# Kernel optimization log

Hardware: AMD Instinct MI355X
Metric: run time of the kernel (lower is better)

Reference implementation:

```python
import jax, jax.numpy as jnp
import numpy as np

N_NODES = 100000
K_STEPS = 10
ALPHA = 0.1


def setup_inputs() -> dict:
    key = jax.random.key(0)
    k1, k2, k3, k4 = jax.random.split(key, 4)
    x = jax.random.normal(k1, (N_NODES, 512), dtype=jnp.float32)
    edge_index = jax.random.randint(k2, (2, 3200000), 0, N_NODES, dtype=jnp.int64)
    W1 = jax.random.normal(k3, (512, 256), dtype=jnp.float32) * (1.0 / np.sqrt(512))
    b1 = jnp.zeros((256,), dtype=jnp.float32)
    W2 = jax.random.normal(k4, (256, 64), dtype=jnp.float32) * (1.0 / np.sqrt(256))
    b2 = jnp.zeros((64,), dtype=jnp.float32)
    return {"x": x, "edge_index": edge_index, "W1": W1, "b1": b1, "W2": W2, "b2": b2}


def _gcn_norm(edge_index, num_nodes):
    # Add self loops and compute symmetric normalization deg^-1/2 A deg^-1/2.
    loops = jnp.arange(num_nodes, dtype=edge_index.dtype)
    src = jnp.concatenate([edge_index[0], loops])
    dst = jnp.concatenate([edge_index[1], loops])
    deg = jax.ops.segment_sum(jnp.ones_like(dst, dtype=jnp.float32), dst,
                              num_segments=num_nodes)
    dinv = jnp.where(deg > 0, jax.lax.rsqrt(deg), 0.0)
    norm = dinv[src] * dinv[dst]  # [E + N]
    return src, dst, norm


def reference(x, edge_index, W1, b1, W2, b2):
    n = x.shape[0]
    # MLP (dropout is identity at inference)
    h = jax.nn.relu(x @ W1 + b1)
    h = h @ W2 + b2  # [N, C]
    # APPNP propagation: h_{k+1} = (1-alpha) * A_hat h_k + alpha * h_0
    src, dst, norm = _gcn_norm(edge_index, n)
    h0 = h

    def step(carry, _):
        msg = carry[src] * norm[:, None]                     # gather + scale
        agg = jax.ops.segment_sum(msg, dst, num_segments=n)  # scatter-add
        return (1.0 - ALPHA) * agg + ALPHA * h0, None

    h, _ = jax.lax.scan(step, h, None, length=K_STEPS)
    return jax.nn.log_softmax(h, axis=1)
```

## Files before the change

kernel.cpp:

```cpp
#include <hip/hip_runtime.h>
#include <cstdint>
#include <cstddef>


typedef _Float16 half8 __attribute__((ext_vector_type(8)));
typedef float floatx4 __attribute__((ext_vector_type(4)));

__device__ inline float2 unpack2(uint u) {
    union { uint u; _Float16 h[2]; } c; c.u = u;
    return make_float2((float)c.h[0], (float)c.h[1]);
}
__device__ inline uint pack2(float a, float b) {
    union { uint u; _Float16 h[2]; } c; c.h[0] = (_Float16)a; c.h[1] = (_Float16)b;
    return c.u;
}

__global__ void transpose_w1(const float* __restrict__ W1, _Float16* __restrict__ W1t) {
    int i = blockIdx.x * 256 + threadIdx.x;
    if (i < 512 * 256) {
        int k = i >> 8, c = i & 255;
        W1t[(size_t)c * 512 + k] = (_Float16)W1[i];
    }
}
__global__ void transpose_w2(const float* __restrict__ W2, _Float16* __restrict__ W2t) {
    int i = blockIdx.x * 256 + threadIdx.x;
    if (i < 256 * 64) {
        int k = i >> 6, c = i & 63;
        W2t[(size_t)c * 256 + k] = (_Float16)W2[i];
    }
}

__global__ __launch_bounds__(256) void mlp_kernel(
    const float* __restrict__ x, const _Float16* __restrict__ W1t,
    const float* __restrict__ b1, const _Float16* __restrict__ W2t,
    const float* __restrict__ b2, _Float16* __restrict__ h0h, int n)
{
    __shared__ __align__(16) _Float16 xs[32][520];
    __shared__ __align__(16) _Float16 hmid[32][264];

    const int tid  = threadIdx.x;
    const int lane = tid & 63;
    const int wid  = tid >> 6;
    const int r0blk = blockIdx.x * 32;
    const int lr = lane & 15;
    const int lg = lane >> 4;

    for (int fi = tid; fi < 32 * 128; fi += 256) {
        int r = fi >> 7, k4 = (fi & 127) * 4;
        float4 v = *(const float4*)(x + (size_t)(r0blk + r) * 512 + k4);
        union { short4 s; _Float16 h[4]; } c;
        c.h[0] = (_Float16)v.x; c.h[1] = (_Float16)v.y;
        c.h[2] = (_Float16)v.z; c.h[3] = (_Float16)v.w;
        *(short4*)&xs[r][k4] = c.s;
    }
    __syncthreads();

    const int wr = wid >> 1, wc = wid & 1;
    floatx4 acc1[8];
#pragma unroll
    for (int ct = 0; ct < 8; ++ct) {
        float b = b1[wc * 128 + ct * 16 + lr];
        acc1[ct] = (floatx4){b, b, b, b};
    }

#pragma unroll 2
    for (int kk = 0; kk < 512; kk += 32) {
        half8 a = *(const half8*)&xs[wr * 16 + lr][kk + lg * 8];
        half8 bfr[8];
#pragma unroll
        for (int ct = 0; ct < 8; ++ct)
            bfr[ct] = *(const half8*)&W1t[(size_t)(wc * 128 + ct * 16 + lr) * 512 + kk + lg * 8];
#pragma unroll
        for (int ct = 0; ct < 8; ++ct)
            acc1[ct] = __builtin_amdgcn_mfma_f32_16x16x32_f16(a, bfr[ct], acc1[ct], 0, 0, 0);
    }

#pragma unroll
    for (int ct = 0; ct < 8; ++ct) {
#pragma unroll
        for (int r = 0; r < 4; ++r) {
            float v = fmaxf(acc1[ct][r], 0.f);
            hmid[wr * 16 + lg * 4 + r][wc * 128 + ct * 16 + lr] = (_Float16)v;
        }
    }
    __syncthreads();

    const int rt = wid >> 1, ct2 = (wid & 1) * 2;
    floatx4 acc2[2] = {(floatx4){0,0,0,0}, (floatx4){0,0,0,0}};
#pragma unroll 2
    for (int kk = 0; kk < 256; kk += 32) {
        half8 a = *(const half8*)&hmid[rt * 16 + lr][kk + lg * 8];
#pragma unroll
        for (int q = 0; q < 2; ++q) {
            half8 b = *(const half8*)&W2t[(size_t)((ct2 + q) * 16 + lr) * 256 + kk + lg * 8];
            acc2[q] = __builtin_amdgcn_mfma_f32_16x16x32_f16(a, b, acc2[q], 0, 0, 0);
        }
    }
#pragma unroll
    for (int q = 0; q < 2; ++q) {
        int col = (ct2 + q) * 16 + lr;
        float bb = b2[col];
#pragma unroll
        for (int r = 0; r < 4; ++r) {
            int row = r0blk + rt * 16 + lg * 4 + r;
            h0h[(size_t)row * 64 + col] = (_Float16)(acc2[q][r] + bb);
        }
    }
}

__global__ void init_counts_kernel(int* __restrict__ counts, int n) {
    int i = blockIdx.x * blockDim.x + threadIdx.x;
    if (i < n) counts[i] = 1;
}

__global__ void count_kernel(const int* __restrict__ dstL, int* __restrict__ counts,
                             int e, int rs, int n) {
    const int r = blockIdx.x & 7;
    const int g = blockIdx.x >> 3;
    const int B = gridDim.x >> 3;
    const int lo = r * rs;
    const int hi = min(lo + rs, n);
    for (int i = g * blockDim.x + threadIdx.x; i < e; i += B * blockDim.x) {
        int d = dstL[i];
        if (d >= lo && d < hi) atomicAdd(&counts[d], 1);
    }
}

__global__ void dinv_kernel(const int* __restrict__ counts, float* __restrict__ dinv, int n) {
    int i = blockIdx.x * blockDim.x + threadIdx.x;
    if (i < n) dinv[i] = 1.0f / sqrtf((float)counts[i]);
}

__global__ __launch_bounds__(256) void scan_a(const int* __restrict__ counts,
                                              int* __restrict__ rowptr,
                                              int* __restrict__ bsums, int n)
{
    __shared__ int s[256];
    const int t = threadIdx.x;
    const int i = blockIdx.x * 256 + t;
    int v = (i < n) ? (counts[i] - 1) : 0;
    s[t] = v;
    __syncthreads();
    for (int off = 1; off < 256; off <<= 1) {
        int add = (t >= off) ? s[t - off] : 0;
        __syncthreads();
        s[t] += add;
        __syncthreads();
    }
    if (i < n) rowptr[i] = s[t] - v;
    if (t == 255) bsums[blockIdx.x] = s[255];
}

__global__ __launch_bounds__(512) void scan_b(const int* __restrict__ bsums,
                                              int* __restrict__ boff, int nb)
{
    __shared__ int s[512];
    const int t = threadIdx.x;
    int v = (t < nb) ? bsums[t] : 0;
    s[t] = v;
    __syncthreads();
    for (int off = 1; off < 512; off <<= 1) {
        int add = (t >= off) ? s[t - off] : 0;
        __syncthreads();
        s[t] += add;
        __syncthreads();
    }
    if (t < nb) boff[t] = s[t] - v;
}

__global__ __launch_bounds__(256) void scan_c(int* __restrict__ rowptr,
                                              int* __restrict__ cursor,
                                              const int* __restrict__ boff, int n, int e)
{
    int i = blockIdx.x * 256 + threadIdx.x;
    if (i < n) {
        int v = rowptr[i] + boff[blockIdx.x];
        rowptr[i] = v;
        cursor[i] = v;
    }
    if (i == 0) rowptr[n] = e;
}

__global__ void fill_kernel(const int* __restrict__ srcL, const int* __restrict__ dstL,
                            int* __restrict__ cursor, int* __restrict__ srcs,
                            int e, int rs, int n) {
    const int r = blockIdx.x & 7;
    const int g = blockIdx.x >> 3;
    const int B = gridDim.x >> 3;
    const int lo = r * rs;
    const int hi = min(lo + rs, n);
    for (int i = g * blockDim.x + threadIdx.x; i < e; i += B * blockDim.x) {
        int d = dstL[i];
        if (d >= lo && d < hi) {
            int pos = atomicAdd(&cursor[d], 1);
            srcs[pos] = srcL[i];
        }
    }
}

__global__ __launch_bounds__(256) void prop_kernel(
    const uint* __restrict__ hu, const uint* __restrict__ h0u,
    uint* __restrict__ hnu, const int* __restrict__ rowptr,
    const int* __restrict__ srcs, const float* __restrict__ dinv, int n)
{
    const int node = (blockIdx.x * blockDim.x + threadIdx.x) >> 6;
    if (node >= n) return;
    const int lane = threadIdx.x & 63;
    const int half_ = lane >> 5;
    const int p = lane & 31;
    const int e0 = rowptr[node], e1 = rowptr[node + 1];
    float accx = 0.f, accy = 0.f;
    int e = e0 + half_;
    for (; e + 6 < e1; e += 8) {
        int s0 = srcs[e], s1 = srcs[e + 2], s2 = srcs[e + 4], s3 = srcs[e + 6];
        float w0 = dinv[s0], w1 = dinv[s1], w2 = dinv[s2], w3 = dinv[s3];
        float2 f0 = unpack2(hu[(size_t)s0 * 32 + p]);
        float2 f1 = unpack2(hu[(size_t)s1 * 32 + p]);
        float2 f2 = unpack2(hu[(size_t)s2 * 32 + p]);
        float2 f3 = unpack2(hu[(size_t)s3 * 32 + p]);
        accx += w0 * f0.x; accy += w0 * f0.y;
        accx += w1 * f1.x; accy += w1 * f1.y;
        accx += w2 * f2.x; accy += w2 * f2.y;
        accx += w3 * f3.x; accy += w3 * f3.y;
    }
    for (; e < e1; e += 2) {
        int s = srcs[e];
        float w = dinv[s];
        float2 f = unpack2(hu[(size_t)s * 32 + p]);
        accx += w * f.x; accy += w * f.y;
    }
    accx += __shfl_xor(accx, 32);
    accy += __shfl_xor(accy, 32);

    const float di = dinv[node];
    float2 self = unpack2(hu[(size_t)node * 32 + p]);
    float2 anc  = unpack2(h0u[(size_t)node * 32 + p]);
    float ox = 0.9f * (di * accx + self.x * di * di) + 0.1f * anc.x;
    float oy = 0.9f * (di * accy + self.y * di * di) + 0.1f * anc.y;
    if (half_ == 0) hnu[(size_t)node * 32 + p] = pack2(ox, oy);
}

__global__ __launch_bounds__(256) void logsoftmax_kernel(
    const _Float16* __restrict__ h, float* __restrict__ out, int n)
{
    const int row = (blockIdx.x * blockDim.x + threadIdx.x) >> 6;
    const int lane = threadIdx.x & 63;
    if (row >= n) return;
    float v = (float)h[(size_t)row * 64 + lane];
    float m = v;
#pragma unroll
    for (int o = 32; o > 0; o >>= 1) m = fmaxf(m, __shfl_xor(m, o));
    float ex = expf(v - m);
    float s = ex;
#pragma unroll
    for (int o = 32; o > 0; o >>= 1) s += __shfl_xor(s, o);
    out[(size_t)row * 64 + lane] = v - m - logf(s);
}

extern "C" void kernel_launch(void* const* d_in, const int* in_sizes, int n_in,
                              void* d_out, int out_size, void* d_ws, size_t ws_size,
                              hipStream_t stream)
{
    const float* x  = (const float*)d_in[0];
    const int*   ei = (const int*)d_in[1];
    const float* W1 = (const float*)d_in[2];
    const float* b1 = (const float*)d_in[3];
    const float* W2 = (const float*)d_in[4];
    const float* b2 = (const float*)d_in[5];
    float* out = (float*)d_out;

    const int n = in_sizes[0] / 512;
    const int e = in_sizes[1] / 2;
    const int* srcL = ei;
    const int* dstL = ei + e;

    char* wsb = (char*)d_ws;
    size_t off = 0;
    auto alloc = [&](size_t bytes) -> void* {
        void* p = wsb + off;
        off = (off + bytes + 255) & ~(size_t)255;
        return p;
    };
    _Float16* h0h = (_Float16*)alloc((size_t)n * 64 * 2);
    _Float16* hp0 = (_Float16*)alloc((size_t)n * 64 * 2);
    _Float16* hp1 = (_Float16*)alloc((size_t)n * 64 * 2);
    int*   srcs   = (int*)alloc((size_t)e * 4);
    float* dinv   = (float*)alloc((size_t)n * 4);
    int*   counts = (int*)alloc((size_t)n * 4);
    int*   rowptr = (int*)alloc((size_t)(n + 1) * 4);
    int*   bsums  = (int*)alloc(4096);
    int*   boff   = (int*)alloc(4096);
    _Float16* W1t = (_Float16*)alloc((size_t)512 * 256 * 2);
    _Float16* W2t = (_Float16*)alloc((size_t)256 * 64 * 2);
    int* cursor = counts;

    const int nb = (n + 255) / 256;
    const int rs = (n + 7) / 8;

    transpose_w1<<<(512 * 256 + 255) / 256, 256, 0, stream>>>(W1, W1t);
    transpose_w2<<<(256 * 64 + 255) / 256, 256, 0, stream>>>(W2, W2t);

    mlp_kernel<<<n / 32, 256, 0, stream>>>(x, W1t, b1, W2t, b2, h0h, n);

    init_counts_kernel<<<nb, 256, 0, stream>>>(counts, n);
    count_kernel<<<1024, 256, 0, stream>>>(dstL, counts, e, rs, n);
    dinv_kernel<<<nb, 256, 0, stream>>>(counts, dinv, n);
    scan_a<<<nb, 256, 0, stream>>>(counts, rowptr, bsums, n);
    scan_b<<<1, 512, 0, stream>>>(bsums, boff, nb);
    scan_c<<<nb, 256, 0, stream>>>(rowptr, cursor, boff, n, e);
    fill_kernel<<<1024, 256, 0, stream>>>(srcL, dstL, cursor, srcs, e, rs, n);

    const int pgrid = (n * 64 + 255) / 256;
    const uint* hin = (const uint*)h0h;
    uint* bufs[2] = {(uint*)hp0, (uint*)hp1};
    for (int it = 0; it < 10; ++it) {
        uint* hn = bufs[it & 1];
        prop_kernel<<<pgrid, 256, 0, stream>>>(hin, (const uint*)h0h, hn,
                                               rowptr, srcs, dinv, n);
        hin = hn;
    }
    logsoftmax_kernel<<<pgrid, 256, 0, stream>>>((const _Float16*)hin, out, n);
}
```

Baseline: 1.588 ms.

## Propagate dinv-scaled features to drop per-edge dinv gathers; stage W1 through LDS

Reformulates the propagation in terms of g = D^{-1/2} h, so each edge contributes an unweighted sum and the per-edge dinv[src] gather goes away. A per-node coefficient 0.9/deg is precomputed, the MLP output is prescaled by dinv, and logsoftmax divides by dinv to recover h. The MLP kernel now streams W1 in a pre-tiled layout through double-buffered shared memory instead of reading it straight from global memory. This requires moving the MLP after the degree computation, and storing the scaled values in fp16 may change rounding behaviour.

Result: faster. 1.445 ms (-9.0%).

```diff
diff --git a/kernel.cpp b/kernel.cpp
--- a/kernel.cpp
+++ b/kernel.cpp
@@ -15,11 +15,11 @@
     return c.u;
 }
 
-__global__ void transpose_w1(const float* __restrict__ W1, _Float16* __restrict__ W1t) {
+__global__ void transpose_w1_tiled(const float* __restrict__ W1, _Float16* __restrict__ W1tt) {
     int i = blockIdx.x * 256 + threadIdx.x;
     if (i < 512 * 256) {
-        int k = i >> 8, c = i & 255;
-        W1t[(size_t)c * 512 + k] = (_Float16)W1[i];
+        int kt = i >> 13, c = (i >> 5) & 255, j = i & 31;
+        W1tt[i] = (_Float16)W1[(size_t)(kt * 32 + j) * 256 + c];
     }
 }
 __global__ void transpose_w2(const float* __restrict__ W2, _Float16* __restrict__ W2t) {
@@ -31,12 +31,13 @@
 }
 
 __global__ __launch_bounds__(256) void mlp_kernel(
-    const float* __restrict__ x, const _Float16* __restrict__ W1t,
+    const float* __restrict__ x, const _Float16* __restrict__ W1tt,
     const float* __restrict__ b1, const _Float16* __restrict__ W2t,
-    const float* __restrict__ b2, _Float16* __restrict__ h0h, int n)
+    const float* __restrict__ b2, const float* __restrict__ dinv,
+    _Float16* __restrict__ g0h, int n)
 {
     __shared__ __align__(16) _Float16 xs[32][520];
-    __shared__ __align__(16) _Float16 hmid[32][264];
+    __shared__ __align__(16) _Float16 wraw[2][10240];
 
     const int tid  = threadIdx.x;
     const int lane = tid & 63;
@@ -53,7 +54,6 @@
         c.h[2] = (_Float16)v.z; c.h[3] = (_Float16)v.w;
         *(short4*)&xs[r][k4] = c.s;
     }
-    __syncthreads();
 
     const int wr = wid >> 1, wc = wid & 1;
     floatx4 acc1[8];
@@ -63,18 +63,45 @@
         acc1[ct] = (floatx4){b, b, b, b};
     }
 
-#pragma unroll 2
-    for (int kk = 0; kk < 512; kk += 32) {
-        half8 a = *(const half8*)&xs[wr * 16 + lr][kk + lg * 8];
-        half8 bfr[8];
-#pragma unroll
-        for (int ct = 0; ct < 8; ++ct)
-            bfr[ct] = *(const half8*)&W1t[(size_t)(wc * 128 + ct * 16 + lr) * 512 + kk + lg * 8];
-#pragma unroll
-        for (int ct = 0; ct < 8; ++ct)
-            acc1[ct] = __builtin_amdgcn_mfma_f32_16x16x32_f16(a, bfr[ct], acc1[ct], 0, 0, 0);
-    }
-
+    const int sc = tid >> 2, ss = (tid & 3) * 8;
+    int4 st0, st1, st2, st3;
+    {
+        const int4* gs = (const int4*)(W1tt);
+        st0 = gs[tid]; st1 = gs[tid + 256]; st2 = gs[tid + 512]; st3 = gs[tid + 768];
+    }
+    {
+        _Float16* wb = wraw[0];
+        *(int4*)&wb[(sc +   0) * 40 + ss] = st0;
+        *(int4*)&wb[(sc +  64) * 40 + ss] = st1;
+        *(int4*)&wb[(sc + 128) * 40 + ss] = st2;
+        *(int4*)&wb[(sc + 192) * 40 + ss] = st3;
+    }
+    __syncthreads();
+
+    for (int kt = 0; kt < 16; ++kt) {
+        const int cur = kt & 1;
+        if (kt < 15) {
+            const int4* gs = (const int4*)(W1tt + (size_t)(kt + 1) * 8192);
+            st0 = gs[tid]; st1 = gs[tid + 256]; st2 = gs[tid + 512]; st3 = gs[tid + 768];
+        }
+        const _Float16* wb = wraw[cur];
+        half8 a = *(const half8*)&xs[wr * 16 + lr][kt * 32 + lg * 8];
+#pragma unroll
+        for (int ct = 0; ct < 8; ++ct) {
+            half8 b = *(const half8*)&wb[(wc * 128 + ct * 16 + lr) * 40 + lg * 8];
+            acc1[ct] = __builtin_amdgcn_mfma_f32_16x16x32_f16(a, b, acc1[ct], 0, 0, 0);
+        }
+        if (kt < 15) {
+            _Float16* wn = wraw[cur ^ 1];
+            *(int4*)&wn[(sc +   0) * 40 + ss] = st0;
+            *(int4*)&wn[(sc +  64) * 40 + ss] = st1;
+            *(int4*)&wn[(sc + 128) * 40 + ss] = st2;
+            *(int4*)&wn[(sc + 192) * 40 + ss] = st3;
+        }
+        __syncthreads();
+    }
+
+    _Float16 (*hmid)[264] = (_Float16(*)[264])&wraw[0][0];
 #pragma unroll
     for (int ct = 0; ct < 8; ++ct) {
 #pragma unroll
@@ -103,7 +130,8 @@
 #pragma unroll
         for (int r = 0; r < 4; ++r) {
             int row = r0blk + rt * 16 + lg * 4 + r;
-            h0h[(size_t)row * 64 + col] = (_Float16)(acc2[q][r] + bb);
+            float di = dinv[row];
+            g0h[(size_t)row * 64 + col] = (_Float16)(di * (acc2[q][r] + bb));
         }
     }
 }
@@ -126,9 +154,14 @@
     }
 }
 
-__global__ void dinv_kernel(const int* __restrict__ counts, float* __restrict__ dinv, int n) {
+__global__ void dinv_kernel(const int* __restrict__ counts, float* __restrict__ dinv,
+                            float* __restrict__ Anode, int n) {
     int i = blockIdx.x * blockDim.x + threadIdx.x;
-    if (i < n) dinv[i] = 1.0f / sqrtf((float)counts[i]);
+    if (i < n) {
+        float deg = (float)counts[i];
+        dinv[i] = 1.0f / sqrtf(deg);
+        Anode[i] = 0.9f / deg;
+    }
 }
 
 __global__ __launch_bounds__(256) void scan_a(const int* __restrict__ counts,
@@ -199,9 +232,9 @@
 }
 
 __global__ __launch_bounds__(256) void prop_kernel(
-    const uint* __restrict__ hu, const uint* __restrict__ h0u,
-    uint* __restrict__ hnu, const int* __restrict__ rowptr,
-    const int* __restrict__ srcs, const float* __restrict__ dinv, int n)
+    const uint* __restrict__ gu, const uint* __restrict__ g0u,
+    uint* __restrict__ gnu, const int* __restrict__ rowptr,
+    const int* __restrict__ srcs, const float* __restrict__ Anode, int n)
 {
     const int node = (blockIdx.x * blockDim.x + threadIdx.x) >> 6;
     if (node >= n) return;
@@ -213,40 +246,38 @@
     int e = e0 + half_;
     for (; e + 6 < e1; e += 8) {
         int s0 = srcs[e], s1 = srcs[e + 2], s2 = srcs[e + 4], s3 = srcs[e + 6];
-        float w0 = dinv[s0], w1 = dinv[s1], w2 = dinv[s2], w3 = dinv[s3];
-        float2 f0 = unpack2(hu[(size_t)s0 * 32 + p]);
-        float2 f1 = unpack2(hu[(size_t)s1 * 32 + p]);
-        float2 f2 = unpack2(hu[(size_t)s2 * 32 + p]);
-        float2 f3 = unpack2(hu[(size_t)s3 * 32 + p]);
-        accx += w0 * f0.x; accy += w0 * f0.y;
-        accx += w1 * f1.x; accy += w1 * f1.y;
-        accx += w2 * f2.x; accy += w2 * f2.y;
-        accx += w3 * f3.x; accy += w3 * f3.y;
+        float2 f0 = unpack2(gu[(size_t)s0 * 32 + p]);
+        float2 f1 = unpack2(gu[(size_t)s1 * 32 + p]);
+        float2 f2 = unpack2(gu[(size_t)s2 * 32 + p]);
+        float2 f3 = unpack2(gu[(size_t)s3 * 32 + p]);
+        accx += f0.x; accy += f0.y;
+        accx += f1.x; accy += f1.y;
+        accx += f2.x; accy += f2.y;
+        accx += f3.x; accy += f3.y;
     }
     for (; e < e1; e += 2) {
-        int s = srcs[e];
-        float w = dinv[s];
-        float2 f = unpack2(hu[(size_t)s * 32 + p]);
-        accx += w * f.x; accy += w * f.y;
+        float2 f = unpack2(gu[(size_t)srcs[e] * 32 + p]);
+        accx += f.x; accy += f.y;
     }
     accx += __shfl_xor(accx, 32);
     accy += __shfl_xor(accy, 32);
 
-    const float di = dinv[node];
-    float2 self = unpack2(hu[(size_t)node * 32 + p]);
-    float2 anc  = unpack2(h0u[(size_t)node * 32 + p]);
-    float ox = 0.9f * (di * accx + self.x * di * di) + 0.1f * anc.x;
-    float oy = 0.9f * (di * accy + self.y * di * di) + 0.1f * anc.y;
-    if (half_ == 0) hnu[(size_t)node * 32 + p] = pack2(ox, oy);
+    const float A = Anode[node];
+    float2 self = unpack2(gu[(size_t)node * 32 + p]);
+    float2 anc  = unpack2(g0u[(size_t)node * 32 + p]);
+    float ox = A * (accx + self.x) + 0.1f * anc.x;
+    float oy = A * (accy + self.y) + 0.1f * anc.y;
+    if (half_ == 0) gnu[(size_t)node * 32 + p] = pack2(ox, oy);
 }
 
 __global__ __launch_bounds__(256) void logsoftmax_kernel(
-    const _Float16* __restrict__ h, float* __restrict__ out, int n)
+    const _Float16* __restrict__ g, const float* __restrict__ dinv,
+    float* __restrict__ out, int n)
 {
     const int row = (blockIdx.x * blockDim.x + threadIdx.x) >> 6;
     const int lane = threadIdx.x & 63;
     if (row >= n) return;
-    float v = (float)h[(size_t)row * 64 + lane];
+    float v = (float)g[(size_t)row * 64 + lane] / dinv[row];
     float m = v;
 #pragma unroll
     for (int o = 32; o > 0; o >>= 1) m = fmaxf(m, __shfl_xor(m, o));
@@ -281,43 +312,44 @@
         off = (off + bytes + 255) & ~(size_t)255;
         return p;
     };
-    _Float16* h0h = (_Float16*)alloc((size_t)n * 64 * 2);
-    _Float16* hp0 = (_Float16*)alloc((size_t)n * 64 * 2);
-    _Float16* hp1 = (_Float16*)alloc((size_t)n * 64 * 2);
+    _Float16* g0h = (_Float16*)alloc((size_t)n * 64 * 2);
+    _Float16* gp0 = (_Float16*)alloc((size_t)n * 64 * 2);
+    _Float16* gp1 = (_Float16*)alloc((size_t)n * 64 * 2);
     int*   srcs   = (int*)alloc((size_t)e * 4);
     float* dinv   = (float*)alloc((size_t)n * 4);
+    float* Anode  = (float*)alloc((size_t)n * 4);
     int*   counts = (int*)alloc((size_t)n * 4);
     int*   rowptr = (int*)alloc((size_t)(n + 1) * 4);
     int*   bsums  = (int*)alloc(4096);
     int*   boff   = (int*)alloc(4096);
-    _Float16* W1t = (_Float16*)alloc((size_t)512 * 256 * 2);
-    _Float16* W2t = (_Float16*)alloc((size_t)256 * 64 * 2);
+    _Float16* W1tt = (_Float16*)alloc((size_t)512 * 256 * 2);
+    _Float16* W2t  = (_Float16*)alloc((size_t)256 * 64 * 2);
     int* cursor = counts;
 
     const int nb = (n + 255) / 256;
     const int rs = (n + 7) / 8;
 
-    transpose_w1<<<(512 * 256 + 255) / 256, 256, 0, stream>>>(W1, W1t);
+    transpose_w1_tiled<<<(512 * 256 + 255) / 256, 256, 0, stream>>>(W1, W1tt);
     transpose_w2<<<(256 * 64 + 255) / 256, 256, 0, stream>>>(W2, W2t);
-
-    mlp_kernel<<<n / 32, 256, 0, stream>>>(x, W1t, b1, W2t, b2, h0h, n);
 
     init_counts_kernel<<<nb, 256, 0, stream>>>(counts, n);
     count_kernel<<<1024, 256, 0, stream>>>(dstL, counts, e, rs, n);
-    dinv_kernel<<<nb, 256, 0, stream>>>(counts, dinv, n);
+    dinv_kernel<<<nb, 256, 0, stream>>>(counts, dinv, Anode, n);
     scan_a<<<nb, 256, 0, stream>>>(counts, rowptr, bsums, n);
     scan_b<<<1, 512, 0, stream>>>(bsums, boff, nb);
     scan_c<<<nb, 256, 0, stream>>>(rowptr, cursor, boff, n, e);
     fill_kernel<<<1024, 256, 0, stream>>>(srcL, dstL, cursor, srcs, e, rs, n);
 
+    mlp_kernel<<<n / 32, 256, 0, stream>>>(x, W1tt, b1, W2t, b2, dinv, g0h, n);
+
     const int pgrid = (n * 64 + 255) / 256;
-    const uint* hin = (const uint*)h0h;
-    uint* bufs[2] = {(uint*)hp0, (uint*)hp1};
+    const uint* gin = (const uint*)g0h;
+    uint* bufs[2] = {(uint*)gp0, (uint*)gp1};
     for (int it = 0; it < 10; ++it) {
-        uint* hn = bufs[it & 1];
-        prop_kernel<<<pgrid, 256, 0, stream>>>(hin, (const uint*)h0h, hn,
-                                               rowptr, srcs, dinv, n);
-        hin = hn;
-    }
-    logsoftmax_kernel<<<pgrid, 256, 0, stream>>>((const _Float16*)hin, out, n);
-}
+        uint* gn = bufs[it & 1];
+        prop_kernel<<<pgrid, 256, 0, stream>>>(gin, (const uint*)g0h, gn,
+                                               rowptr, srcs, Anode, n);
+        gin = gn;
+    }
+    logsoftmax_kernel<<<pgrid, 256, 0, stream>>>((const _Float16*)gin, dinv, out, n);
+}
```
